# Optimization experiments

Hardware: AMD Instinct MI355X
Metric: run time of the kernel (lower is better)

## Reference

```python
import jax, jax.numpy as jnp
import numpy as np

PS = 8
NUM_HEADS = 8

def _rel_pos_index(ps):
    # identical to the torch buffer construction in __init__
    coords = np.stack(np.meshgrid(np.arange(ps), np.arange(ps), indexing='ij'))  # [2,ps,ps]
    cf = coords.reshape(2, -1)                       # [2, N]
    rel = cf[:, :, None] - cf[:, None, :]            # [2, N, N]
    rel = rel.transpose(1, 2, 0).copy()              # [N, N, 2]
    rel[:, :, 0] += ps - 1
    rel[:, :, 1] += ps - 1
    rel[:, :, 0] *= 2 * ps - 1
    return jnp.asarray(rel.sum(-1))                  # [N, N] int


def setup_inputs() -> dict:
    key = jax.random.key(0)
    ks = jax.random.split(key, 8)
    t, h, w, c = 4, 256, 256, 256
    s = 1.0 / np.sqrt(c).astype(np.float32)
    return {
        'vid': jax.random.normal(ks[0], (t, h, w, c), jnp.float32),
        'modulator': jax.random.normal(ks[1], (PS * PS, c), jnp.float32) * 0.02,
        'wq': jax.random.normal(ks[2], (c, c), jnp.float32) * s,
        'bq': jnp.zeros((c,), jnp.float32),
        'wkv': jax.random.normal(ks[3], (c, 2 * c), jnp.float32) * s,
        'bkv': jnp.zeros((2 * c,), jnp.float32),
        'proj_w': jax.random.normal(ks[4], (c, c), jnp.float32) * s,
        'proj_b': jnp.zeros((c,), jnp.float32),
        'rel_pos_table': jax.random.normal(ks[5], ((2 * PS - 1) ** 2, NUM_HEADS), jnp.float32) * 0.02,
    }


def reference(vid, modulator, wq, bq, wkv, bkv, proj_w, proj_b, rel_pos_table):
    t, h, w, c = vid.shape
    ps, nh = PS, NUM_HEADS
    hd = c // nh
    scale = hd ** (-0.5)
    N = ps * ps
    # extract ps x ps windows -> [nwin, N, c]
    x = vid.reshape(t, h // ps, ps, w // ps, ps, c)
    x = x.transpose(0, 1, 3, 2, 4, 5).reshape(-1, N, c)
    x = x + modulator[None]                          # per-patch modulator weight
    q = x @ wq + bq                                  # [nwin, N, c]
    kv = x @ wkv + bkv                               # [nwin, N, 2c]
    k, v = kv[..., :c], kv[..., c:]
    heads = lambda a: a.reshape(-1, N, nh, hd).transpose(0, 2, 1, 3)  # [nwin, nh, N, hd]
    q, k, v = heads(q) * scale, heads(k), heads(v)
    rpi = _rel_pos_index(ps)
    bias = rel_pos_table[rpi.reshape(-1)].reshape(N, N, nh).transpose(2, 0, 1)  # [nh, N, N]
    attn = jnp.einsum('nhqd,nhkd->nhqk', q, k) + bias[None]
    attn = jax.nn.softmax(attn, axis=-1)
    out = jnp.einsum('nhqk,nhkd->nhqd', attn, v)
    out = out.transpose(0, 2, 1, 3).reshape(-1, N, c)
    out = out @ proj_w + proj_b
    out = out.reshape(t, h // ps, w // ps, ps, ps, c)
    out = out.transpose(0, 1, 3, 2, 4, 5).reshape(t, h, w, c)
    return out
```

## Files before the change

### kernel.cpp

```cpp
#include <hip/hip_runtime.h>

typedef __bf16 bf16x8 __attribute__((ext_vector_type(8)));
typedef __bf16 bf16x4 __attribute__((ext_vector_type(4)));
typedef float  f32x4  __attribute__((ext_vector_type(4)));

#define MFMA(A,B,C) __builtin_amdgcn_mfma_f32_16x16x32_bf16((A),(B),(C),0,0,0)
#define LDS_FENCE() do { asm volatile("s_waitcnt lgkmcnt(0)" ::: "memory"); \
                         __builtin_amdgcn_sched_barrier(0); } while (0)


constexpr int XS_STRIDE = 264;
constexpr int SC_STRIDE = 72;
constexpr int OFF_XO  = 0;
constexpr int OFF_SC  = 33792;
constexpr int LDS_BYTES = 43008;

__global__ void prep_weights(const float* __restrict__ wq,
                             const float* __restrict__ wkv,
                             const float* __restrict__ projw,
                             __bf16* __restrict__ wfrag)
{
    const int lane = threadIdx.x & 63;
    const int kt   = threadIdx.x >> 6;
    const int ct   = blockIdx.x;
    const int nl   = lane & 15;
    const int kk0  = kt * 32 + ((lane >> 4) << 3);
    __bf16* dst = wfrag + (((size_t)ct * 8 + kt) * 64 + lane) * 8;
    bf16x8 o;
#pragma unroll
    for (int j = 0; j < 8; ++j) {
        const int kk = kk0 + j;
        float v;
        if (ct < 16)       v = wq  [kk * 256 +             ct        * 16 + nl];
        else if (ct < 32)  v = wkv [kk * 512 +             (ct - 16) * 16 + nl];
        else if (ct < 48)  v = wkv [kk * 512 + 256 +       (ct - 32) * 16 + nl];
        else               v = projw[kk * 256 +            (ct - 48) * 16 + nl];
        o[j] = (__bf16)v;
    }
    *(bf16x8*)dst = o;
}

__global__ void prep_bias(const float* __restrict__ table, float* __restrict__ biasf)
{
    const int g    = blockIdx.x * 256 + threadIdx.x;
    const int lane = g & 63;
    const int nt   = (g >> 6) & 3;
    const int mt   = (g >> 8) & 3;
    const int h    = g >> 10;
    const int colL = lane & 15;
    const int rowC = (lane >> 4) << 2;
    const int k     = nt * 16 + colL;
    const int kcode = (k >> 3) * 15 + (k & 7);
    f32x4 o;
#pragma unroll
    for (int r = 0; r < 4; ++r) {
        const int q     = mt * 16 + rowC + r;
        const int qcode = (q >> 3) * 15 + (q & 7) + 112;
        o[r] = table[(qcode - kcode) * 8 + h];
    }
    ((f32x4*)biasf)[g] = o;
}

__global__ __launch_bounds__(256, 3)
void attn_fused(const float* __restrict__ vid,
                const float* __restrict__ mod,
                const float* __restrict__ bq,
                const float* __restrict__ bkv,
                const float* __restrict__ projb,
                const float* __restrict__ biasf,
                const __bf16* __restrict__ wfrag,
                float* __restrict__ out)
{
    extern __shared__ char smem[];
    __bf16* s_xo = (__bf16*)(smem + OFF_XO);
    __bf16* s_tl = (__bf16*)(smem + OFF_SC) + (threadIdx.x >> 6) * (16 * SC_STRIDE);

    const int tid  = threadIdx.x;
    const int lane = tid & 63;
    const int wv   = tid >> 6;
    const int colL = lane & 15;
    const int quad = lane >> 4;
    const int kq   = quad << 3;
    const int rowC = quad << 2;

    const int b  = blockIdx.x;
    const int tt = b >> 10;
    const int wy = (b >> 5) & 31;
    const int wx = b & 31;
    const int base0 = tt * (1 << 24) + wy * 8 * 65536 + wx * 8 * 256;

#pragma unroll
    for (int i = 0; i < 16; ++i) {
        const int idx = tid + 256 * i;
        const int m  = idx >> 6;
        const int c4 = (idx & 63) << 2;
        const int py = m >> 3, px = m & 7;
        const float4 xv = *(const float4*)(vid + base0 + py * 65536 + px * 256 + c4);
        const float4 mv = *(const float4*)(mod + m * 256 + c4);
        bf16x4 o;
        o[0] = (__bf16)(xv.x + mv.x);
        o[1] = (__bf16)(xv.y + mv.y);
        o[2] = (__bf16)(xv.z + mv.z);
        o[3] = (__bf16)(xv.w + mv.w);
        *(bf16x4*)&s_xo[m * XS_STRIDE + c4] = o;
    }
    __syncthreads();

    bf16x8 aq[2][4];
    bf16x8 bk[2][4];
    bf16x8 bv[2][2][2];

    auto gemm16 = [&](int part, const float* __restrict__ bias_p, f32x4 (&acc)[4][4]) {
        float bias[4];
#pragma unroll
        for (int ntl = 0; ntl < 4; ++ntl)
            bias[ntl] = bias_p[(wv * 4 + ntl) * 16 + colL];
#pragma unroll
        for (int ntl = 0; ntl < 4; ++ntl)
#pragma unroll
            for (int mt = 0; mt < 4; ++mt)
                acc[ntl][mt] = {bias[ntl], bias[ntl], bias[ntl], bias[ntl]};
        const int ct0 = part * 16 + wv * 4;
#pragma unroll
        for (int kt = 0; kt < 8; ++kt) {
            bf16x8 a[4];
#pragma unroll
            for (int mt = 0; mt < 4; ++mt)
                a[mt] = *(const bf16x8*)&s_xo[(mt * 16 + colL) * XS_STRIDE + kt * 32 + kq];
#pragma unroll
            for (int ntl = 0; ntl < 4; ++ntl) {
                const bf16x8 bf =
                    *((const bf16x8*)wfrag + ((size_t)(ct0 + ntl) * 8 + kt) * 64 + lane);
#pragma unroll
                for (int mt = 0; mt < 4; ++mt)
                    acc[ntl][mt] = MFMA(a[mt], bf, acc[ntl][mt]);
            }
        }
    };

    const float SCALE = 0.17677669529663687f;

    {
        f32x4 acc[4][4];
        gemm16(0, bq, acc);
#pragma unroll
        for (int mt = 0; mt < 4; ++mt) {
#pragma unroll
            for (int ntl = 0; ntl < 4; ++ntl)
#pragma unroll
                for (int r = 0; r < 4; ++r)
                    s_tl[(rowC + r) * SC_STRIDE + ntl * 16 + colL] =
                        (__bf16)(acc[ntl][mt][r] * SCALE);
            LDS_FENCE();
#pragma unroll
            for (int hh = 0; hh < 2; ++hh)
                aq[hh][mt] = *(const bf16x8*)&s_tl[colL * SC_STRIDE + hh * 32 + kq];
            LDS_FENCE();
        }
    }

    {
        f32x4 acc[4][4];
        gemm16(1, bkv, acc);
#pragma unroll
        for (int nt = 0; nt < 4; ++nt) {
#pragma unroll
            for (int ntl = 0; ntl < 4; ++ntl)
#pragma unroll
                for (int r = 0; r < 4; ++r)
                    s_tl[(rowC + r) * SC_STRIDE + ntl * 16 + colL] = (__bf16)acc[ntl][nt][r];
            LDS_FENCE();
#pragma unroll
            for (int hh = 0; hh < 2; ++hh)
                bk[hh][nt] = *(const bf16x8*)&s_tl[colL * SC_STRIDE + hh * 32 + kq];
            LDS_FENCE();
        }
    }

    {
        f32x4 acc[4][4];
        gemm16(2, bkv + 256, acc);
#pragma unroll
        for (int ntl = 0; ntl < 4; ++ntl) {
#pragma unroll
            for (int mt = 0; mt < 4; ++mt) {
                bf16x4 o;
                o[0] = (__bf16)acc[ntl][mt][0]; o[1] = (__bf16)acc[ntl][mt][1];
                o[2] = (__bf16)acc[ntl][mt][2]; o[3] = (__bf16)acc[ntl][mt][3];
                *(bf16x4*)&s_tl[colL * SC_STRIDE + mt * 16 + rowC] = o;
            }
            LDS_FENCE();
            const int hh = ntl >> 1, n2 = ntl & 1;
#pragma unroll
            for (int k2 = 0; k2 < 2; ++k2)
                bv[hh][n2][k2] = *(const bf16x8*)&s_tl[colL * SC_STRIDE + k2 * 32 + kq];
            LDS_FENCE();
        }
    }
    __syncthreads();

    const f32x4* __restrict__ bfr = (const f32x4*)biasf;
#pragma unroll
    for (int hh = 0; hh < 2; ++hh) {
        const int h = 2 * wv + hh;
        f32x4 S[4][4];
#pragma unroll
        for (int mt = 0; mt < 4; ++mt)
#pragma unroll
            for (int nt = 0; nt < 4; ++nt)
                S[mt][nt] = MFMA(aq[hh][mt], bk[hh][nt],
                                 bfr[((h * 4 + mt) * 4 + nt) * 64 + lane]);

#pragma unroll
        for (int mt = 0; mt < 4; ++mt)
#pragma unroll
            for (int r = 0; r < 4; ++r) {
                float mx = S[mt][0][r];
#pragma unroll
                for (int nt = 1; nt < 4; ++nt) mx = fmaxf(mx, S[mt][nt][r]);
                mx = fmaxf(mx, __shfl_xor(mx, 1));
                mx = fmaxf(mx, __shfl_xor(mx, 2));
                mx = fmaxf(mx, __shfl_xor(mx, 4));
                mx = fmaxf(mx, __shfl_xor(mx, 8));
                float sum = 0.f;
#pragma unroll
                for (int nt = 0; nt < 4; ++nt) {
                    const float e = __expf(S[mt][nt][r] - mx);
                    S[mt][nt][r] = e;
                    sum += e;
                }
                sum += __shfl_xor(sum, 1);
                sum += __shfl_xor(sum, 2);
                sum += __shfl_xor(sum, 4);
                sum += __shfl_xor(sum, 8);
                const float inv = 1.0f / sum;
#pragma unroll
                for (int nt = 0; nt < 4; ++nt) S[mt][nt][r] *= inv;
            }

#pragma unroll
        for (int mt = 0; mt < 4; ++mt) {
#pragma unroll
            for (int nt = 0; nt < 4; ++nt)
#pragma unroll
                for (int r = 0; r < 4; ++r)
                    s_tl[(rowC + r) * SC_STRIDE + nt * 16 + colL] = (__bf16)S[mt][nt][r];
            LDS_FENCE();
            const bf16x8 ap0 = *(const bf16x8*)&s_tl[colL * SC_STRIDE + kq];
            const bf16x8 ap1 = *(const bf16x8*)&s_tl[colL * SC_STRIDE + 32 + kq];
            LDS_FENCE();
#pragma unroll
            for (int n2 = 0; n2 < 2; ++n2) {
                f32x4 o = {0.f, 0.f, 0.f, 0.f};
                o = MFMA(ap0, bv[hh][n2][0], o);
                o = MFMA(ap1, bv[hh][n2][1], o);
#pragma unroll
                for (int r = 0; r < 4; ++r)
                    s_xo[(mt * 16 + rowC + r) * XS_STRIDE + h * 32 + n2 * 16 + colL] =
                        (__bf16)o[r];
            }
        }
    }
    __syncthreads();

    {
        f32x4 acc[4][4];
        gemm16(3, projb, acc);
#pragma unroll
        for (int ntl = 0; ntl < 4; ++ntl) {
            const int n = (wv * 4 + ntl) * 16 + colL;
#pragma unroll
            for (int mt = 0; mt < 4; ++mt)
#pragma unroll
                for (int r = 0; r < 4; ++r) {
                    const int m = mt * 16 + rowC + r;
                    out[base0 + (m >> 3) * 65536 + (m & 7) * 256 + n] = acc[ntl][mt][r];
                }
        }
    }
}

extern "C" void kernel_launch(void* const* d_in, const int* in_sizes, int n_in,
                              void* d_out, int out_size, void* d_ws, size_t ws_size,
                              hipStream_t stream)
{
    const float* vid  = (const float*)d_in[0];
    const float* mod  = (const float*)d_in[1];
    const float* wq   = (const float*)d_in[2];
    const float* bq   = (const float*)d_in[3];
    const float* wkv  = (const float*)d_in[4];
    const float* bkv  = (const float*)d_in[5];
    const float* pw   = (const float*)d_in[6];
    const float* pb   = (const float*)d_in[7];
    const float* tab  = (const float*)d_in[8];
    __bf16* wfrag = (__bf16*)d_ws;
    float*  biasf = (float*)((char*)d_ws + 524288);

    prep_weights<<<64, 512, 0, stream>>>(wq, wkv, pw, wfrag);
    prep_bias<<<32, 256, 0, stream>>>(tab, biasf);

    (void)hipFuncSetAttribute((const void*)attn_fused,
                              hipFuncAttributeMaxDynamicSharedMemorySize, LDS_BYTES);
    attn_fused<<<4096, 256, LDS_BYTES, stream>>>(vid, mod, bq, bkv, pb, biasf, wfrag,
                                                 (float*)d_out);
}
```

Baseline: 744.7 us.

## Use 512-thread blocks with one head per wave and XOR-swizzled LDS

Doubles the workgroup to 8 waves so each wave owns a single attention head and computes only its 32-column slices of the Q, K, V and projection GEMMs, which cuts per-wave register pressure and accumulator arrays. The padded LDS strides are replaced by XOR-swizzled addressing to avoid bank conflicts without padding, and the launch bounds are changed to allow more resident waves. The trade-off is more waves competing for LDS and a larger LDS footprint per block (48 KB), which could lower the number of blocks per CU.

```diff
diff --git a/kernel.cpp b/kernel.cpp
--- a/kernel.cpp
+++ b/kernel.cpp
@@ -9,11 +9,16 @@
                          __builtin_amdgcn_sched_barrier(0); } while (0)
 
 
-constexpr int XS_STRIDE = 264;
-constexpr int SC_STRIDE = 72;
-constexpr int OFF_XO  = 0;
-constexpr int OFF_SC  = 33792;
-constexpr int LDS_BYTES = 43008;
+constexpr int OFF_XO = 0;
+constexpr int OFF_SC = 32768;
+constexpr int LDS_BYTES = 49152;
+
+__device__ __forceinline__ int xo_addr(int row, int col) {
+    return (row * 512 + col * 2) ^ ((row & 7) << 4);
+}
+__device__ __forceinline__ int sc_addr(int row, int col) {
+    return (row * 128 + col * 2) ^ ((row & 7) << 4);
+}
 
 __global__ void prep_weights(const float* __restrict__ wq,
                              const float* __restrict__ wkv,
@@ -61,7 +66,7 @@
     ((f32x4*)biasf)[g] = o;
 }
 
-__global__ __launch_bounds__(256, 3)
+__global__ __launch_bounds__(512, 4)
 void attn_fused(const float* __restrict__ vid,
                 const float* __restrict__ mod,
                 const float* __restrict__ bq,
@@ -72,8 +77,8 @@
                 float* __restrict__ out)
 {
     extern __shared__ char smem[];
-    __bf16* s_xo = (__bf16*)(smem + OFF_XO);
-    __bf16* s_tl = (__bf16*)(smem + OFF_SC) + (threadIdx.x >> 6) * (16 * SC_STRIDE);
+    char* xo = smem + OFF_XO;
+    char* sc = smem + OFF_SC + (threadIdx.x >> 6) * 2048;
 
     const int tid  = threadIdx.x;
     const int lane = tid & 63;
@@ -82,6 +87,7 @@
     const int quad = lane >> 4;
     const int kq   = quad << 3;
     const int rowC = quad << 2;
+    const int h    = wv;
 
     const int b  = blockIdx.x;
     const int tt = b >> 10;
@@ -90,8 +96,8 @@
     const int base0 = tt * (1 << 24) + wy * 8 * 65536 + wx * 8 * 256;
 
 #pragma unroll
-    for (int i = 0; i < 16; ++i) {
-        const int idx = tid + 256 * i;
+    for (int i = 0; i < 8; ++i) {
+        const int idx = tid + 512 * i;
         const int m  = idx >> 6;
         const int c4 = (idx & 63) << 2;
         const int py = m >> 3, px = m & 7;
@@ -102,98 +108,95 @@
         o[1] = (__bf16)(xv.y + mv.y);
         o[2] = (__bf16)(xv.z + mv.z);
         o[3] = (__bf16)(xv.w + mv.w);
-        *(bf16x4*)&s_xo[m * XS_STRIDE + c4] = o;
+        *(bf16x4*)(xo + xo_addr(m, c4)) = o;
     }
     __syncthreads();
 
-    bf16x8 aq[2][4];
-    bf16x8 bk[2][4];
-    bf16x8 bv[2][2][2];
-
-    auto gemm16 = [&](int part, const float* __restrict__ bias_p, f32x4 (&acc)[4][4]) {
-        float bias[4];
-#pragma unroll
-        for (int ntl = 0; ntl < 4; ++ntl)
-            bias[ntl] = bias_p[(wv * 4 + ntl) * 16 + colL];
-#pragma unroll
-        for (int ntl = 0; ntl < 4; ++ntl)
-#pragma unroll
-            for (int mt = 0; mt < 4; ++mt)
-                acc[ntl][mt] = {bias[ntl], bias[ntl], bias[ntl], bias[ntl]};
-        const int ct0 = part * 16 + wv * 4;
+    auto gemm2 = [&](int ct0, const float* __restrict__ bias_p, f32x4 (&acc)[2][4]) {
+        const float b0 = bias_p[colL], b1 = bias_p[16 + colL];
+#pragma unroll
+        for (int mt = 0; mt < 4; ++mt) {
+            acc[0][mt] = {b0, b0, b0, b0};
+            acc[1][mt] = {b1, b1, b1, b1};
+        }
 #pragma unroll
         for (int kt = 0; kt < 8; ++kt) {
             bf16x8 a[4];
 #pragma unroll
             for (int mt = 0; mt < 4; ++mt)
-                a[mt] = *(const bf16x8*)&s_xo[(mt * 16 + colL) * XS_STRIDE + kt * 32 + kq];
-#pragma unroll
-            for (int ntl = 0; ntl < 4; ++ntl) {
+                a[mt] = *(const bf16x8*)(xo + xo_addr(mt * 16 + colL, kt * 32 + kq));
+#pragma unroll
+            for (int n = 0; n < 2; ++n) {
                 const bf16x8 bf =
-                    *((const bf16x8*)wfrag + ((size_t)(ct0 + ntl) * 8 + kt) * 64 + lane);
+                    *((const bf16x8*)wfrag + ((size_t)(ct0 + n) * 8 + kt) * 64 + lane);
 #pragma unroll
                 for (int mt = 0; mt < 4; ++mt)
-                    acc[ntl][mt] = MFMA(a[mt], bf, acc[ntl][mt]);
+                    acc[n][mt] = MFMA(a[mt], bf, acc[n][mt]);
             }
         }
     };
 
     const float SCALE = 0.17677669529663687f;
+    bf16x8 aq[4], bk[4], bv[2][2];
 
     {
-        f32x4 acc[4][4];
-        gemm16(0, bq, acc);
-#pragma unroll
-        for (int mt = 0; mt < 4; ++mt) {
-#pragma unroll
-            for (int ntl = 0; ntl < 4; ++ntl)
-#pragma unroll
-                for (int r = 0; r < 4; ++r)
-                    s_tl[(rowC + r) * SC_STRIDE + ntl * 16 + colL] =
-                        (__bf16)(acc[ntl][mt][r] * SCALE);
-            LDS_FENCE();
-#pragma unroll
-            for (int hh = 0; hh < 2; ++hh)
-                aq[hh][mt] = *(const bf16x8*)&s_tl[colL * SC_STRIDE + hh * 32 + kq];
-            LDS_FENCE();
-        }
-    }
-
-    {
-        f32x4 acc[4][4];
-        gemm16(1, bkv, acc);
-#pragma unroll
-        for (int nt = 0; nt < 4; ++nt) {
-#pragma unroll
-            for (int ntl = 0; ntl < 4; ++ntl)
-#pragma unroll
-                for (int r = 0; r < 4; ++r)
-                    s_tl[(rowC + r) * SC_STRIDE + ntl * 16 + colL] = (__bf16)acc[ntl][nt][r];
-            LDS_FENCE();
-#pragma unroll
-            for (int hh = 0; hh < 2; ++hh)
-                bk[hh][nt] = *(const bf16x8*)&s_tl[colL * SC_STRIDE + hh * 32 + kq];
-            LDS_FENCE();
-        }
-    }
-
-    {
-        f32x4 acc[4][4];
-        gemm16(2, bkv + 256, acc);
-#pragma unroll
-        for (int ntl = 0; ntl < 4; ++ntl) {
+        f32x4 acc[2][4];
+        gemm2(32 + 2 * h, bkv + 256 + h * 32, acc);
+#pragma unroll
+        for (int n = 0; n < 2; ++n) {
 #pragma unroll
             for (int mt = 0; mt < 4; ++mt) {
                 bf16x4 o;
-                o[0] = (__bf16)acc[ntl][mt][0]; o[1] = (__bf16)acc[ntl][mt][1];
-                o[2] = (__bf16)acc[ntl][mt][2]; o[3] = (__bf16)acc[ntl][mt][3];
-                *(bf16x4*)&s_tl[colL * SC_STRIDE + mt * 16 + rowC] = o;
+                o[0] = (__bf16)acc[n][mt][0]; o[1] = (__bf16)acc[n][mt][1];
+                o[2] = (__bf16)acc[n][mt][2]; o[3] = (__bf16)acc[n][mt][3];
+                *(bf16x4*)(sc + sc_addr(colL, mt * 16 + rowC)) = o;
             }
             LDS_FENCE();
-            const int hh = ntl >> 1, n2 = ntl & 1;
 #pragma unroll
             for (int k2 = 0; k2 < 2; ++k2)
-                bv[hh][n2][k2] = *(const bf16x8*)&s_tl[colL * SC_STRIDE + k2 * 32 + kq];
+                bv[n][k2] = *(const bf16x8*)(sc + sc_addr(colL, k2 * 32 + kq));
+            LDS_FENCE();
+        }
+    }
+
+    {
+        f32x4 acc[2][4];
+        gemm2(2 * h, bq + h * 32, acc);
+#pragma unroll
+        for (int g = 0; g < 2; ++g) {
+#pragma unroll
+            for (int t = 0; t < 2; ++t)
+#pragma unroll
+                for (int n = 0; n < 2; ++n)
+#pragma unroll
+                    for (int r = 0; r < 4; ++r)
+                        *(__bf16*)(sc + sc_addr(rowC + r, t * 32 + n * 16 + colL)) =
+                            (__bf16)(acc[n][2 * g + t][r] * SCALE);
+            LDS_FENCE();
+#pragma unroll
+            for (int t = 0; t < 2; ++t)
+                aq[2 * g + t] = *(const bf16x8*)(sc + sc_addr(colL, t * 32 + kq));
+            LDS_FENCE();
+        }
+    }
+
+    {
+        f32x4 acc[2][4];
+        gemm2(16 + 2 * h, bkv + h * 32, acc);
+#pragma unroll
+        for (int g = 0; g < 2; ++g) {
+#pragma unroll
+            for (int t = 0; t < 2; ++t)
+#pragma unroll
+                for (int n = 0; n < 2; ++n)
+#pragma unroll
+                    for (int r = 0; r < 4; ++r)
+                        *(__bf16*)(sc + sc_addr(rowC + r, t * 32 + n * 16 + colL)) =
+                            (__bf16)acc[n][2 * g + t][r];
+            LDS_FENCE();
+#pragma unroll
+            for (int t = 0; t < 2; ++t)
+                bk[2 * g + t] = *(const bf16x8*)(sc + sc_addr(colL, t * 32 + kq));
             LDS_FENCE();
         }
     }
@@ -201,23 +204,22 @@
 
     const f32x4* __restrict__ bfr = (const f32x4*)biasf;
 #pragma unroll
-    for (int hh = 0; hh < 2; ++hh) {
-        const int h = 2 * wv + hh;
-        f32x4 S[4][4];
-#pragma unroll
-        for (int mt = 0; mt < 4; ++mt)
+    for (int H = 0; H < 2; ++H) {
+        f32x4 S[2][4];
+#pragma unroll
+        for (int m = 0; m < 2; ++m)
 #pragma unroll
             for (int nt = 0; nt < 4; ++nt)
-                S[mt][nt] = MFMA(aq[hh][mt], bk[hh][nt],
-                                 bfr[((h * 4 + mt) * 4 + nt) * 64 + lane]);
-
-#pragma unroll
-        for (int mt = 0; mt < 4; ++mt)
+                S[m][nt] = MFMA(aq[2 * H + m], bk[nt],
+                                bfr[((h * 4 + 2 * H + m) * 4 + nt) * 64 + lane]);
+
+#pragma unroll
+        for (int m = 0; m < 2; ++m)
 #pragma unroll
             for (int r = 0; r < 4; ++r) {
-                float mx = S[mt][0][r];
-#pragma unroll
-                for (int nt = 1; nt < 4; ++nt) mx = fmaxf(mx, S[mt][nt][r]);
+                float mx = S[m][0][r];
+#pragma unroll
+                for (int nt = 1; nt < 4; ++nt) mx = fmaxf(mx, S[m][nt][r]);
                 mx = fmaxf(mx, __shfl_xor(mx, 1));
                 mx = fmaxf(mx, __shfl_xor(mx, 2));
                 mx = fmaxf(mx, __shfl_xor(mx, 4));
@@ -225,8 +227,8 @@
                 float sum = 0.f;
 #pragma unroll
                 for (int nt = 0; nt < 4; ++nt) {
-                    const float e = __expf(S[mt][nt][r] - mx);
-                    S[mt][nt][r] = e;
+                    const float e = __expf(S[m][nt][r] - mx);
+                    S[m][nt][r] = e;
                     sum += e;
                 }
                 sum += __shfl_xor(sum, 1);
@@ -235,46 +237,46 @@
                 sum += __shfl_xor(sum, 8);
                 const float inv = 1.0f / sum;
 #pragma unroll
-                for (int nt = 0; nt < 4; ++nt) S[mt][nt][r] *= inv;
+                for (int nt = 0; nt < 4; ++nt) S[m][nt][r] *= inv;
             }
 
 #pragma unroll
-        for (int mt = 0; mt < 4; ++mt) {
+        for (int m = 0; m < 2; ++m) {
 #pragma unroll
             for (int nt = 0; nt < 4; ++nt)
 #pragma unroll
                 for (int r = 0; r < 4; ++r)
-                    s_tl[(rowC + r) * SC_STRIDE + nt * 16 + colL] = (__bf16)S[mt][nt][r];
-            LDS_FENCE();
-            const bf16x8 ap0 = *(const bf16x8*)&s_tl[colL * SC_STRIDE + kq];
-            const bf16x8 ap1 = *(const bf16x8*)&s_tl[colL * SC_STRIDE + 32 + kq];
+                    *(__bf16*)(sc + sc_addr(rowC + r, nt * 16 + colL)) = (__bf16)S[m][nt][r];
+            LDS_FENCE();
+            const bf16x8 ap0 = *(const bf16x8*)(sc + sc_addr(colL, kq));
+            const bf16x8 ap1 = *(const bf16x8*)(sc + sc_addr(colL, 32 + kq));
             LDS_FENCE();
 #pragma unroll
             for (int n2 = 0; n2 < 2; ++n2) {
                 f32x4 o = {0.f, 0.f, 0.f, 0.f};
-                o = MFMA(ap0, bv[hh][n2][0], o);
-                o = MFMA(ap1, bv[hh][n2][1], o);
+                o = MFMA(ap0, bv[n2][0], o);
+                o = MFMA(ap1, bv[n2][1], o);
 #pragma unroll
                 for (int r = 0; r < 4; ++r)
-                    s_xo[(mt * 16 + rowC + r) * XS_STRIDE + h * 32 + n2 * 16 + colL] =
-                        (__bf16)o[r];
+                    *(__bf16*)(xo + xo_addr((2 * H + m) * 16 + rowC + r,
+                                            h * 32 + n2 * 16 + colL)) = (__bf16)o[r];
             }
         }
     }
     __syncthreads();
 
     {
-        f32x4 acc[4][4];
-        gemm16(3, projb, acc);
-#pragma unroll
-        for (int ntl = 0; ntl < 4; ++ntl) {
-            const int n = (wv * 4 + ntl) * 16 + colL;
+        f32x4 acc[2][4];
+        gemm2(48 + 2 * wv, projb + wv * 32, acc);
+#pragma unroll
+        for (int n = 0; n < 2; ++n) {
+            const int nn = wv * 32 + n * 16 + colL;
 #pragma unroll
             for (int mt = 0; mt < 4; ++mt)
 #pragma unroll
                 for (int r = 0; r < 4; ++r) {
                     const int m = mt * 16 + rowC + r;
-                    out[base0 + (m >> 3) * 65536 + (m & 7) * 256 + n] = acc[ntl][mt][r];
+                    out[base0 + (m >> 3) * 65536 + (m & 7) * 256 + nn] = acc[n][mt][r];
                 }
         }
     }
@@ -301,6 +303,6 @@
 
     (void)hipFuncSetAttribute((const void*)attn_fused,
                               hipFuncAttributeMaxDynamicSharedMemorySize, LDS_BYTES);
-    attn_fused<<<4096, 256, LDS_BYTES, stream>>>(vid, mod, bq, bkv, pb, biasf, wfrag,
+    attn_fused<<<4096, 512, LDS_BYTES, stream>>>(vid, mod, bq, bkv, pb, biasf, wfrag,
                                                  (float*)d_out);
 }
```

After: 768.5 us. 3.2% more time.
